# Optimization experiments

Hardware: AMD Instinct MI355X
Metric: run time of the kernel (lower is better)

The kernel has to match this reference:

```python
import jax, jax.numpy as jnp
import numpy as np


def setup_inputs() -> dict:
    key = jax.random.key(0)
    kW, kH, kT = jax.random.split(key, 3)
    N, M, rank = 1024, 1024, 64
    W = jax.random.uniform(kW, (N, rank), dtype=jnp.float32)
    H = jax.random.uniform(kH, (rank, M), dtype=jnp.float32)
    tau = jax.random.uniform(kT, (N, rank), dtype=jnp.float32)
    return {"W": W, "H": H, "tau": tau}


def reference(W, H, tau):
    # Vectorized ShiftNMF forward over all M frequency bins at once.
    # Original: for f in range(M): WHt[:, f] = (softplus(W) * exp(-1j*2*pi*f/M * tau)) @ Hf[:, f]
    M = H.shape[1]
    Hf = jnp.fft.fft(jax.nn.softplus(H), axis=1)          # (rank, M) complex64
    Wp = jax.nn.softplus(W)                                # (N, rank)
    freqs = jnp.arange(M, dtype=jnp.float32)               # (M,)
    # phase[n, r, f] = exp(-1j * 2*pi*f/M * tau[n, r])
    phase = jnp.exp((-2j * jnp.pi / M) * tau[:, :, None] * freqs[None, None, :])  # (N, rank, M)
    # WHt[n, f] = sum_r Wp[n, r] * phase[n, r, f] * Hf[r, f]
    WHt = jnp.einsum('nr,nrf,rf->nf', Wp.astype(phase.dtype), phase, Hf)
    return WHt
```

## Files before the change

kernel.cpp:

```cpp
#include <hip/hip_runtime.h>
#include <math.h>

#define M_DIM 1024
#define N_DIM 1024
#define NRANK 64
#define BN 16
#define BF 64

__device__ float g_HfRe[NRANK * M_DIM];
__device__ float g_HfIm[NRANK * M_DIM];

__device__ __forceinline__ float softplus_f(float x) {
    return log1pf(__expf(x));
}

__device__ __forceinline__ float fast_sin_rev(float rev) {
#if __has_builtin(__builtin_amdgcn_sinf)
    return __builtin_amdgcn_sinf(rev);
#else
    return __sinf(rev * 6.28318530717958647f);
#endif
}
__device__ __forceinline__ float fast_cos_rev(float rev) {
#if __has_builtin(__builtin_amdgcn_cosf)
    return __builtin_amdgcn_cosf(rev);
#else
    return __cosf(rev * 6.28318530717958647f);
#endif
}

__global__ __launch_bounds__(512) void fft_rows(const float* __restrict__ H) {
    __shared__ float sre[M_DIM];
    __shared__ float sim[M_DIM];
    const int r = blockIdx.x;
    const int tid = threadIdx.x;

    for (int j = tid; j < M_DIM; j += 512) {
        int src = __brev((unsigned)j) >> 22;
        sre[j] = softplus_f(H[r * M_DIM + src]);
        sim[j] = 0.0f;
    }
    __syncthreads();

    int log2half = 0;
    for (int len = 2; len <= M_DIM; len <<= 1, ++log2half) {
        const int half = len >> 1;
        const int j    = tid & (half - 1);
        const int base = (tid >> log2half) << (log2half + 1);
        const int i0   = base + j;
        const int i1   = i0 + half;
        const float rev = -(float)j / (float)len;
        const float s = fast_sin_rev(rev);
        const float c = fast_cos_rev(rev);
        const float xr = sre[i1], xi = sim[i1];
        const float vr = xr * c - xi * s;
        const float vi = xr * s + xi * c;
        const float ur = sre[i0], ui = sim[i0];
        sre[i0] = ur + vr;  sim[i0] = ui + vi;
        sre[i1] = ur - vr;  sim[i1] = ui - vi;
        __syncthreads();
    }

    for (int j = tid; j < M_DIM; j += 512) {
        g_HfRe[r * M_DIM + j] = sre[j];
        g_HfIm[r * M_DIM + j] = sim[j];
    }
}

__global__ __launch_bounds__(256) void shiftnmf_main(
    const float* __restrict__ W, const float* __restrict__ tau,
    float* __restrict__ out, int out_elems) {

    __shared__ float shHr[NRANK][BF];
    __shared__ float shHi[NRANK][BF];
    __shared__ float shWp[NRANK][BN];
    __shared__ float shA [NRANK][BN];
    __shared__ float shSc[NRANK][BN];
    __shared__ float shSs[NRANK][BN];

    const int tid = threadIdx.x;
    const int f0  = blockIdx.x * BF;
    const int n0  = blockIdx.y * BN;

    for (int idx = tid; idx < NRANK * BF; idx += 256) {
        const int rr = idx >> 6, ff = idx & 63;
        shHr[rr][ff] = g_HfRe[rr * M_DIM + f0 + ff];
        shHi[rr][ff] = g_HfIm[rr * M_DIM + f0 + ff];
    }
    for (int idx = tid; idx < BN * NRANK; idx += 256) {
        const int nn = idx >> 6, rr = idx & 63;
        const int n  = n0 + nn;
        const float wp = softplus_f(W[n * NRANK + rr]);
        const float a  = (-1.0f / (float)M_DIM) * tau[n * NRANK + rr];
        shWp[rr][nn] = wp;
        shA [rr][nn] = a;
        const float rev16 = a * 16.0f;
        shSc[rr][nn] = fast_cos_rev(rev16);
        shSs[rr][nn] = fast_sin_rev(rev16);
    }
    __syncthreads();

    const int fbase = tid & 15;
    const int n_loc = tid >> 4;
    const float fglob = (float)(f0 + fbase);

    float accRe[4] = {0.f, 0.f, 0.f, 0.f};
    float accIm[4] = {0.f, 0.f, 0.f, 0.f};

    for (int r = 0; r < NRANK; ++r) {
        const float wp  = shWp[r][n_loc];
        const float a   = shA [r][n_loc];
        const float c16 = shSc[r][n_loc];
        const float s16 = shSs[r][n_loc];
        const float rev0 = a * fglob;
        const float s0 = fast_sin_rev(rev0);
        const float c0 = fast_cos_rev(rev0);
        float pr = wp * c0;
        float pi = wp * s0;
        #pragma unroll
        for (int k = 0; k < 4; ++k) {
            const float hr = shHr[r][fbase + (k << 4)];
            const float hi = shHi[r][fbase + (k << 4)];
            accRe[k] = fmaf(pr, hr, fmaf(-pi, hi, accRe[k]));
            accIm[k] = fmaf(pr, hi, fmaf( pi, hr, accIm[k]));
            if (k < 3) {
                const float npr = fmaf(pr, c16, -pi * s16);
                pi = fmaf(pr, s16, pi * c16);
                pr = npr;
            }
        }
    }

    #pragma unroll
    for (int k = 0; k < 4; ++k) {
        const int n  = n0 + n_loc;
        const int oi = n * M_DIM + f0 + fbase + (k << 4);
        if (oi < out_elems) out[oi] = accRe[k];
        const int oj = N_DIM * M_DIM + oi;
        if (oj < out_elems) out[oj] = accIm[k];
    }
}

extern "C" void kernel_launch(void* const* d_in, const int* in_sizes, int n_in,
                              void* d_out, int out_size, void* d_ws, size_t ws_size,
                              hipStream_t stream) {
    const float* W   = (const float*)d_in[0];
    const float* H   = (const float*)d_in[1];
    const float* tau = (const float*)d_in[2];

    (void)d_ws; (void)ws_size;

    fft_rows<<<NRANK, 512, 0, stream>>>(H);
    shiftnmf_main<<<dim3(M_DIM / BF, N_DIM / BN), 256, 0, stream>>>(
        W, tau, (float*)d_out, out_size);
}
```

Before: 87.73 us.

## Interleave complex Hf storage and use packed float2 FMAs in main loop

Stores the FFT output as interleaved complex pairs and packs the per-(r,n) coefficients (a, wp, cos16, sin16) into one padded float4 in shared memory. The inner complex multiply-accumulate is rewritten with two-wide vector FMAs so the compiler can emit packed FP32 instructions. The aim is fewer shared-memory load instructions and fewer FMA issues per output. The cost is extra swizzle/negation operations, and packed-math codegen is not guaranteed.

```diff
diff --git a/kernel.cpp b/kernel.cpp
--- a/kernel.cpp
+++ b/kernel.cpp
@@ -7,8 +7,9 @@
 #define BN 16
 #define BF 64
 
-__device__ float g_HfRe[NRANK * M_DIM];
-__device__ float g_HfIm[NRANK * M_DIM];
+typedef float f32x2 __attribute__((ext_vector_type(2)));
+
+__device__ f32x2 g_Hf[NRANK * M_DIM];
 
 __device__ __forceinline__ float softplus_f(float x) {
     return log1pf(__expf(x));
@@ -62,8 +63,7 @@
     }
 
     for (int j = tid; j < M_DIM; j += 512) {
-        g_HfRe[r * M_DIM + j] = sre[j];
-        g_HfIm[r * M_DIM + j] = sim[j];
+        g_Hf[r * M_DIM + j] = (f32x2){sre[j], sim[j]};
     }
 }
 
@@ -71,12 +71,8 @@
     const float* __restrict__ W, const float* __restrict__ tau,
     float* __restrict__ out, int out_elems) {
 
-    __shared__ float shHr[NRANK][BF];
-    __shared__ float shHi[NRANK][BF];
-    __shared__ float shWp[NRANK][BN];
-    __shared__ float shA [NRANK][BN];
-    __shared__ float shSc[NRANK][BN];
-    __shared__ float shSs[NRANK][BN];
+    __shared__ f32x2  shHf[NRANK][BF];
+    __shared__ float4 shC [NRANK][BN + 1];
 
     const int tid = threadIdx.x;
     const int f0  = blockIdx.x * BF;
@@ -84,19 +80,15 @@
 
     for (int idx = tid; idx < NRANK * BF; idx += 256) {
         const int rr = idx >> 6, ff = idx & 63;
-        shHr[rr][ff] = g_HfRe[rr * M_DIM + f0 + ff];
-        shHi[rr][ff] = g_HfIm[rr * M_DIM + f0 + ff];
+        shHf[rr][ff] = g_Hf[rr * M_DIM + f0 + ff];
     }
     for (int idx = tid; idx < BN * NRANK; idx += 256) {
         const int nn = idx >> 6, rr = idx & 63;
         const int n  = n0 + nn;
         const float wp = softplus_f(W[n * NRANK + rr]);
         const float a  = (-1.0f / (float)M_DIM) * tau[n * NRANK + rr];
-        shWp[rr][nn] = wp;
-        shA [rr][nn] = a;
         const float rev16 = a * 16.0f;
-        shSc[rr][nn] = fast_cos_rev(rev16);
-        shSs[rr][nn] = fast_sin_rev(rev16);
+        shC[rr][nn] = make_float4(a, wp, fast_cos_rev(rev16), fast_sin_rev(rev16));
     }
     __syncthreads();
 
@@ -104,29 +96,24 @@
     const int n_loc = tid >> 4;
     const float fglob = (float)(f0 + fbase);
 
-    float accRe[4] = {0.f, 0.f, 0.f, 0.f};
-    float accIm[4] = {0.f, 0.f, 0.f, 0.f};
+    f32x2 acc[4] = {{0.f, 0.f}, {0.f, 0.f}, {0.f, 0.f}, {0.f, 0.f}};
 
     for (int r = 0; r < NRANK; ++r) {
-        const float wp  = shWp[r][n_loc];
-        const float a   = shA [r][n_loc];
-        const float c16 = shSc[r][n_loc];
-        const float s16 = shSs[r][n_loc];
-        const float rev0 = a * fglob;
-        const float s0 = fast_sin_rev(rev0);
-        const float c0 = fast_cos_rev(rev0);
-        float pr = wp * c0;
-        float pi = wp * s0;
+        const float4 cf = shC[r][n_loc];
+        const float rev0 = cf.x * fglob;
+        f32x2 p;
+        p.x = cf.y * fast_cos_rev(rev0);
+        p.y = cf.y * fast_sin_rev(rev0);
+        const f32x2 st = {cf.z, cf.w};
         #pragma unroll
         for (int k = 0; k < 4; ++k) {
-            const float hr = shHr[r][fbase + (k << 4)];
-            const float hi = shHi[r][fbase + (k << 4)];
-            accRe[k] = fmaf(pr, hr, fmaf(-pi, hi, accRe[k]));
-            accIm[k] = fmaf(pr, hi, fmaf( pi, hr, accIm[k]));
+            const f32x2 h = shHf[r][fbase + (k << 4)];
+            const f32x2 pneg = {-p.y, p.y};
+            acc[k] = __builtin_elementwise_fma(pneg, (f32x2){h.y, h.x}, acc[k]);
+            acc[k] = __builtin_elementwise_fma((f32x2){p.x, p.x}, h, acc[k]);
             if (k < 3) {
-                const float npr = fmaf(pr, c16, -pi * s16);
-                pi = fmaf(pr, s16, pi * c16);
-                pr = npr;
+                const f32x2 t = pneg * (f32x2){st.y, st.x};
+                p = __builtin_elementwise_fma((f32x2){p.x, p.x}, st, t);
             }
         }
     }
@@ -135,9 +122,9 @@
     for (int k = 0; k < 4; ++k) {
         const int n  = n0 + n_loc;
         const int oi = n * M_DIM + f0 + fbase + (k << 4);
-        if (oi < out_elems) out[oi] = accRe[k];
+        if (oi < out_elems) out[oi] = acc[k].x;
         const int oj = N_DIM * M_DIM + oi;
-        if (oj < out_elems) out[oj] = accIm[k];
+        if (oj < out_elems) out[oj] = acc[k].y;
     }
 }
 
```

Measured after the change: 85.12 us. -3.0%, faster.
